# Performance work log

Measured on AMD Instinct MI355X. Metric: run time of the kernel, lower is better.

Reference implementation:

```python
import jax, jax.numpy as jnp
import numpy as np

N = 100000
E = 1600000
D = 256
BN_EPS = 1e-5


def setup_inputs() -> dict:
    key = jax.random.key(0)
    ks = jax.random.split(key, 6)
    node_feats = jax.random.normal(ks[0], (N, D), dtype=jnp.float32)
    src = jax.random.randint(ks[1], (E,), 0, N, dtype=jnp.int64)
    dst = jax.random.randint(ks[2], (E,), 0, N, dtype=jnp.int64)
    eps = jnp.zeros((1,), dtype=jnp.float32)
    # Kaiming-uniform-like scaled init for linear layers
    W1 = jax.random.normal(ks[3], (D, 2 * D), dtype=jnp.float32) * (1.0 / np.sqrt(D))
    b1 = jnp.zeros((2 * D,), dtype=jnp.float32)
    W2 = jax.random.normal(ks[4], (2 * D, D), dtype=jnp.float32) * (1.0 / np.sqrt(2 * D))
    b2 = jnp.zeros((D,), dtype=jnp.float32)
    gamma = jnp.ones((D,), dtype=jnp.float32)
    beta = jnp.zeros((D,), dtype=jnp.float32)
    return {"node_feats": node_feats, "src": src, "dst": dst, "eps": eps,
            "W1": W1, "b1": b1, "W2": W2, "b2": b2, "gamma": gamma, "beta": beta}


def reference(node_feats, src, dst, eps, W1, b1, W2, b2, gamma, beta):
    n = node_feats.shape[0]
    # copy_u / sum: gather source features, scatter-sum into destinations
    neigh = jax.ops.segment_sum(node_feats[src], dst, num_segments=n)  # [N, D]
    h = (1.0 + eps) * node_feats + neigh
    # 2-layer MLP: D -> 2D -> D with ReLU
    h = jax.nn.relu(h @ W1 + b1) @ W2 + b2
    # BatchNorm1d, training mode: batch stats over N, biased variance
    mean = jnp.mean(h, axis=0)
    var = jnp.mean(jnp.square(h - mean), axis=0)
    h = (h - mean) * jax.lax.rsqrt(var + BN_EPS) * gamma + beta
    return h
```

## Files before the change

### kernel.cpp

```cpp
#include <hip/hip_runtime.h>
#include <hip/hip_bf16.h>
#include <stdint.h>

#define N_NODES 100000
#define DIM 256
#define HID 512
#define N_EDGES 1600000

#define NBUCK 782
#define BSHIFT 7
#define BMASK 127
#define CAPC 4096
#define CURSTRIDE 16

using short8 = __attribute__((ext_vector_type(8))) short;
using f32x4  = __attribute__((ext_vector_type(4))) float;

__device__ __forceinline__ unsigned short f2bf(float f) {
    union { float f; unsigned u; } v; v.f = f;
    unsigned u = v.u;
    unsigned r = u + 0x7fffu + ((u >> 16) & 1u);
    return (unsigned short)(r >> 16);
}
__device__ __forceinline__ float bf2f(unsigned short u) {
    union { unsigned u; float f; } v; v.u = ((unsigned)u) << 16; return v.f;
}
__device__ __forceinline__ void gload_lds16(const void* g, void* l) {
    __builtin_amdgcn_global_load_lds((const __attribute__((address_space(1))) void*)g,
                                     (__attribute__((address_space(3))) void*)l, 16, 0, 0);
}

__global__ void x2bf(const float* __restrict__ x, unsigned short* __restrict__ xb) {
    long i = (long)blockIdx.x * blockDim.x + threadIdx.x;
    float4 u0 = ((const float4*)x)[i * 2];
    float4 u1 = ((const float4*)x)[i * 2 + 1];
    short8 o;
    o[0] = (short)f2bf(u0.x); o[1] = (short)f2bf(u0.y);
    o[2] = (short)f2bf(u0.z); o[3] = (short)f2bf(u0.w);
    o[4] = (short)f2bf(u1.x); o[5] = (short)f2bf(u1.y);
    o[6] = (short)f2bf(u1.z); o[7] = (short)f2bf(u1.w);
    ((short8*)xb)[i] = o;
}


__global__ void zero_cursors(int* __restrict__ chunkCursor) {
    int i = blockIdx.x * 256 + threadIdx.x;
    if (i < NBUCK * CURSTRIDE) chunkCursor[i] = 0;
}

__global__ void bucket_scatter(const int* __restrict__ src, const int* __restrict__ dst,
                               int* __restrict__ chunkCursor, int* __restrict__ bucketed) {
    int e = blockIdx.x * 256 + threadIdx.x;
    int d = dst[e];
    int c = d >> BSHIFT;
    int pos = atomicAdd(&chunkCursor[c * CURSTRIDE], 1);
    bucketed[(size_t)c * CAPC + pos] = src[e] | ((d & BMASK) << 17);
}

__global__ void scan_chunks(const int* __restrict__ chunkCursor, int* __restrict__ chunkOff) {
    __shared__ int sm[1024];
    int t = threadIdx.x;
    int v = (t < NBUCK) ? chunkCursor[t * CURSTRIDE] : 0;
    sm[t] = v;
    __syncthreads();
    for (int off = 1; off < 1024; off <<= 1) {
        int add = (t >= off) ? sm[t - off] : 0;
        __syncthreads();
        sm[t] += add;
        __syncthreads();
    }
    chunkOff[t] = sm[t] - v;
}

__global__ __launch_bounds__(256) void chunk_sort(const int* __restrict__ bucketed,
        const int* __restrict__ chunkCursor, const int* __restrict__ chunkOff,
        int* __restrict__ start, int* __restrict__ count, int* __restrict__ sorted_src) {
    __shared__ int cnt[128];
    __shared__ int cur[128];
    __shared__ int sortedL[CAPC];
    int c = blockIdx.x;
    int t = threadIdx.x;
    int nE = chunkCursor[c * CURSTRIDE];
    int base = chunkOff[c];
    const int* bk = bucketed + (size_t)c * CAPC;
    if (t < 128) cnt[t] = 0;
    __syncthreads();
    for (int i = t; i < nE; i += 256)
        atomicAdd(&cnt[bk[i] >> 17], 1);
    __syncthreads();
    int v = (t < 128) ? cnt[t] : 0;
    for (int off = 1; off < 128; off <<= 1) {
        int add = (t >= off && t < 128) ? cnt[t - off] : 0;
        __syncthreads();
        if (t < 128) cnt[t] += add;
        __syncthreads();
    }
    if (t < 128) {
        int excl = cnt[t] - v;
        int gid = c * 128 + t;
        start[gid] = base + excl;
        count[gid] = v;
        cur[t] = excl;
    }
    __syncthreads();
    for (int i = t; i < nE; i += 256) {
        int p = bk[i];
        int pos = atomicAdd(&cur[p >> 17], 1);
        sortedL[pos] = p & 0x1FFFF;
    }
    __syncthreads();
    for (int i = t; i < nE; i += 256)
        sorted_src[base + i] = sortedL[i];
}

__global__ void gather_sum(const unsigned short* __restrict__ xb, const int* __restrict__ sorted_src,
                           const int* __restrict__ start, const int* __restrict__ count,
                           const float* __restrict__ eps, unsigned short* __restrict__ accb) {
    int lane = threadIdx.x & 63;
    int n = blockIdx.x * 4 + (threadIdx.x >> 6);
    if (n >= N_NODES) return;
    float s = 1.0f + eps[0];
    const ushort4* xr = (const ushort4*)(xb + (size_t)n * DIM);
    ushort4 v = xr[lane];
    float a0 = bf2f(v.x) * s, a1 = bf2f(v.y) * s, a2 = bf2f(v.z) * s, a3 = bf2f(v.w) * s;
    int base = start[n];
    int end = base + count[n];
    int j = base;
    for (; j + 4 <= end; j += 4) {
        int s0 = sorted_src[j], s1 = sorted_src[j + 1];
        int s2 = sorted_src[j + 2], s3 = sorted_src[j + 3];
        ushort4 v0 = ((const ushort4*)(xb + (size_t)s0 * DIM))[lane];
        ushort4 v1 = ((const ushort4*)(xb + (size_t)s1 * DIM))[lane];
        ushort4 v2 = ((const ushort4*)(xb + (size_t)s2 * DIM))[lane];
        ushort4 v3 = ((const ushort4*)(xb + (size_t)s3 * DIM))[lane];
        a0 += bf2f(v0.x) + bf2f(v1.x) + bf2f(v2.x) + bf2f(v3.x);
        a1 += bf2f(v0.y) + bf2f(v1.y) + bf2f(v2.y) + bf2f(v3.y);
        a2 += bf2f(v0.z) + bf2f(v1.z) + bf2f(v2.z) + bf2f(v3.z);
        a3 += bf2f(v0.w) + bf2f(v1.w) + bf2f(v2.w) + bf2f(v3.w);
    }
    for (; j < end; ++j) {
        int s0 = sorted_src[j];
        ushort4 v0 = ((const ushort4*)(xb + (size_t)s0 * DIM))[lane];
        a0 += bf2f(v0.x); a1 += bf2f(v0.y); a2 += bf2f(v0.z); a3 += bf2f(v0.w);
    }
    ushort4 o;
    o.x = f2bf(a0); o.y = f2bf(a1); o.z = f2bf(a2); o.w = f2bf(a3);
    ((ushort4*)(accb + (size_t)n * DIM))[lane] = o;
}


__global__ void prep_weights(const float* __restrict__ W1, const float* __restrict__ W2,
                             unsigned short* __restrict__ W1t, unsigned short* __restrict__ W2t) {
    int tid = blockIdx.x * blockDim.x + threadIdx.x;
    if (tid < DIM * HID) {
        int n = tid >> 8, k = tid & 255;
        W1t[tid] = f2bf(W1[k * HID + n]);
    } else {
        int j = tid - DIM * HID;
        int n = j >> 9, k = j & 511;
        W2t[j] = f2bf(W2[k * DIM + n]);
    }
}

template<int K, int NOUT, bool RELU_BF16_OUT>
__global__ __launch_bounds__(256) void gemm128(const unsigned short* __restrict__ A,
        const unsigned short* __restrict__ Bt, const float* __restrict__ bias,
        void* __restrict__ Cout, int M) {
    __shared__ unsigned short As[128 * 32];
    __shared__ unsigned short Bs[128 * 32];
    constexpr int NT = NOUT / 128;
    int mtile = blockIdx.x / NT;
    int ntile = blockIdx.x % NT;
    int mbase = mtile * 128, nbase = ntile * 128;
    int t = threadIdx.x;
    int lane = t & 63, wid = t >> 6;
    int wm = (wid & 1) * 64, wn = (wid >> 1) * 64;
    int lo = lane & 15, quad = lane >> 4;

    int s0 = t, s1 = t + 256;
    int r0 = s0 >> 2, c0 = (s0 & 3) ^ ((r0 >> 1) & 3);
    int r1 = s1 >> 2, c1 = (s1 & 3) ^ ((r1 >> 1) & 3);
    int gmA0 = mbase + r0; if (gmA0 >= M) gmA0 = M - 1;
    int gmA1 = mbase + r1; if (gmA1 >= M) gmA1 = M - 1;
    const unsigned short* gA0 = A + (size_t)gmA0 * K + c0 * 8;
    const unsigned short* gA1 = A + (size_t)gmA1 * K + c1 * 8;
    const unsigned short* gB0 = Bt + (size_t)(nbase + r0) * K + c0 * 8;
    const unsigned short* gB1 = Bt + (size_t)(nbase + r1) * K + c1 * 8;
    char* lA0 = (char*)As + wid * 1024;
    char* lA1 = (char*)As + 4096 + wid * 1024;
    char* lB0 = (char*)Bs + wid * 1024;
    char* lB1 = (char*)Bs + 4096 + wid * 1024;

    int offA[4], offB[4];
    #pragma unroll
    for (int i = 0; i < 4; ++i) {
        int ra = wm + i * 16 + lo;
        offA[i] = ra * 64 + ((quad ^ ((ra >> 1) & 3)) * 16);
        int rb = wn + i * 16 + lo;
        offB[i] = rb * 64 + ((quad ^ ((rb >> 1) & 3)) * 16);
    }

    f32x4 acc[4][4] = {};
    for (int kt = 0; kt < K / 32; ++kt) {
        if (kt) __syncthreads();
        int ko = kt * 32;
        gload_lds16(gA0 + ko, lA0);
        gload_lds16(gA1 + ko, lA1);
        gload_lds16(gB0 + ko, lB0);
        gload_lds16(gB1 + ko, lB1);
        __syncthreads();
        short8 a[4], b[4];
        #pragma unroll
        for (int i = 0; i < 4; ++i) {
            a[i] = *(const short8*)((const char*)As + offA[i]);
            b[i] = *(const short8*)((const char*)Bs + offB[i]);
        }
        #pragma unroll
        for (int mi = 0; mi < 4; ++mi)
            #pragma unroll
            for (int ni = 0; ni < 4; ++ni)
                acc[mi][ni] = __builtin_amdgcn_mfma_f32_16x16x32_bf16(a[mi], b[ni], acc[mi][ni], 0, 0, 0);
    }
    #pragma unroll
    for (int mi = 0; mi < 4; ++mi)
      #pragma unroll
      for (int ni = 0; ni < 4; ++ni)
        #pragma unroll
        for (int r = 0; r < 4; ++r) {
            int row = mbase + wm + mi * 16 + quad * 4 + r;
            int col = nbase + wn + ni * 16 + lo;
            if (row < M) {
                float v = acc[mi][ni][r] + bias[col];
                if constexpr (RELU_BF16_OUT) {
                    v = fmaxf(v, 0.0f);
                    ((unsigned short*)Cout)[(size_t)row * NOUT + col] = f2bf(v);
                } else {
                    ((float*)Cout)[(size_t)row * NOUT + col] = v;
                }
            }
        }
}


__global__ void col_stats1(const float* __restrict__ h, float* __restrict__ partial) {
    int t = threadIdx.x;
    int b = blockIdx.x;
    int r0 = b * 200;
    int r1 = r0 + 200; if (r1 > N_NODES) r1 = N_NODES;
    float s = 0.f, q = 0.f;
    for (int r = r0; r < r1; ++r) {
        float v = h[(size_t)r * DIM + t];
        s += v; q += v * v;
    }
    partial[b * 512 + t] = s;
    partial[b * 512 + 256 + t] = q;
}

__global__ void col_stats2(const float* __restrict__ partial, const float* __restrict__ gamma,
                           const float* __restrict__ beta, float* __restrict__ sc) {
    int t = threadIdx.x;
    float s = 0.f, q = 0.f;
    for (int b = 0; b < 500; ++b) {
        s += partial[b * 512 + t];
        q += partial[b * 512 + 256 + t];
    }
    float mean = s * (1.0f / (float)N_NODES);
    float var = q * (1.0f / (float)N_NODES) - mean * mean;
    float inv = rsqrtf(var + 1e-5f);
    float scale = gamma[t] * inv;
    sc[t] = scale;
    sc[256 + t] = beta[t] - mean * scale;
}

__global__ void bn_apply(const float* __restrict__ h, const float* __restrict__ sc,
                         float* __restrict__ out) {
    long i = (long)blockIdx.x * blockDim.x + threadIdx.x;
    int c = (int)((i * 4) & (DIM - 1));
    float4 v = ((const float4*)h)[i];
    float4 scale = *(const float4*)(sc + c);
    float4 shift = *(const float4*)(sc + 256 + c);
    float4 o;
    o.x = v.x * scale.x + shift.x;
    o.y = v.y * scale.y + shift.y;
    o.z = v.z * scale.z + shift.z;
    o.w = v.w * scale.w + shift.w;
    ((float4*)out)[i] = o;
}

extern "C" void kernel_launch(void* const* d_in, const int* in_sizes, int n_in,
                              void* d_out, int out_size, void* d_ws, size_t ws_size,
                              hipStream_t stream) {
    const float* x     = (const float*)d_in[0];
    const int*   src   = (const int*)d_in[1];
    const int*   dst   = (const int*)d_in[2];
    const float* eps   = (const float*)d_in[3];
    const float* W1    = (const float*)d_in[4];
    const float* b1    = (const float*)d_in[5];
    const float* W2    = (const float*)d_in[6];
    const float* b2    = (const float*)d_in[7];
    const float* gamma = (const float*)d_in[8];
    const float* beta  = (const float*)d_in[9];

    char* ws = (char*)d_ws;
    unsigned short* xb   = (unsigned short*)ws;
    unsigned short* accb = (unsigned short*)(ws + 51200000);
    float*          h2   = (float*)ws;
    unsigned short* W1t  = (unsigned short*)(ws + 102400000);
    unsigned short* W2t  = (unsigned short*)(ws + 102662144);
    float*          sc   = (float*)(ws + 102924288);

    char* ob = (char*)d_out;
    int* chunkCursor = (int*)ob;
    int* chunkOff    = (int*)(ob + 51200);
    int* start       = (int*)(ob + 55296);
    int* count       = (int*)(ob + 455680);
    int* sorted_src  = (int*)(ob + 856064);
    int* bucketed    = (int*)(ob + 7256064);
    unsigned short* tbuf    = (unsigned short*)d_out;
    float*          partial = (float*)d_out;
    float*          out     = (float*)d_out;

    hipLaunchKernelGGL(x2bf, dim3(12500), dim3(256), 0, stream, x, xb);
    hipLaunchKernelGGL(prep_weights, dim3(1024), dim3(256), 0, stream, W1, W2, W1t, W2t);
    hipLaunchKernelGGL(zero_cursors, dim3(49), dim3(256), 0, stream, chunkCursor);
    hipLaunchKernelGGL(bucket_scatter, dim3(N_EDGES / 256), dim3(256), 0, stream,
                       src, dst, chunkCursor, bucketed);
    hipLaunchKernelGGL(scan_chunks, dim3(1), dim3(1024), 0, stream, chunkCursor, chunkOff);
    hipLaunchKernelGGL(chunk_sort, dim3(NBUCK), dim3(256), 0, stream,
                       bucketed, chunkCursor, chunkOff, start, count, sorted_src);
    hipLaunchKernelGGL(gather_sum, dim3(25000), dim3(256), 0, stream,
                       xb, sorted_src, start, count, eps, accb);
    hipLaunchKernelGGL((gemm128<256, 512, true>), dim3(782 * 4), dim3(256), 0, stream,
                       accb, W1t, b1, (void*)tbuf, N_NODES);
    hipLaunchKernelGGL((gemm128<512, 256, false>), dim3(782 * 2), dim3(256), 0, stream,
                       tbuf, W2t, b2, (void*)h2, N_NODES);
    hipLaunchKernelGGL(col_stats1, dim3(500), dim3(256), 0, stream, h2, partial);
    hipLaunchKernelGGL(col_stats2, dim3(1), dim3(256), 0, stream, partial, gamma, beta, sc);
    hipLaunchKernelGGL(bn_apply, dim3(25000), dim3(256), 0, stream, h2, sc, out);
}
```

Baseline: 664.1 us.

## Fuse BatchNorm column stats into second GEMM, persistent gather with sorted sources

Moves the column sum and sum-of-squares reduction into the epilogue of the second GEMM: each block reduces through shuffles and shared-memory atomics, then adds into one of 8 replicated global accumulators. This removes the separate col_stats1 pass that re-read the 100 MB fp32 output. The gather kernel becomes a grid-stride persistent kernel unrolled by 8 to keep more loads in flight. chunk_sort also insertion-sorts each destination's source list, which should improve locality of the gathers but adds serial per-thread work and makes the fp32 atomic column sums order-nondeterministic.

```diff
diff --git a/kernel.cpp b/kernel.cpp
--- a/kernel.cpp
+++ b/kernel.cpp
@@ -43,9 +43,10 @@
 }
 
 
-__global__ void zero_cursors(int* __restrict__ chunkCursor) {
+__global__ void zero_scratch(int* __restrict__ chunkCursor, float* __restrict__ gsums) {
     int i = blockIdx.x * 256 + threadIdx.x;
     if (i < NBUCK * CURSTRIDE) chunkCursor[i] = 0;
+    if (i < 4096) gsums[i] = 0.0f;
 }
 
 __global__ void bucket_scatter(const int* __restrict__ src, const int* __restrict__ dst,
@@ -95,12 +96,14 @@
         if (t < 128) cnt[t] += add;
         __syncthreads();
     }
+    int segs = 0, segc = 0;
     if (t < 128) {
-        int excl = cnt[t] - v;
+        segc = v;
+        segs = cnt[t] - v;
         int gid = c * 128 + t;
-        start[gid] = base + excl;
+        start[gid] = base + segs;
         count[gid] = v;
-        cur[t] = excl;
+        cur[t] = segs;
     }
     __syncthreads();
     for (int i = t; i < nE; i += 256) {
@@ -109,43 +112,72 @@
         sortedL[pos] = p & 0x1FFFF;
     }
     __syncthreads();
+    if (t < 128 && segc > 1) {
+        for (int i = segs + 1; i < segs + segc; ++i) {
+            int key = sortedL[i];
+            int k = i - 1;
+            while (k >= segs && sortedL[k] > key) { sortedL[k + 1] = sortedL[k]; --k; }
+            sortedL[k + 1] = key;
+        }
+    }
+    __syncthreads();
     for (int i = t; i < nE; i += 256)
         sorted_src[base + i] = sortedL[i];
 }
 
-__global__ void gather_sum(const unsigned short* __restrict__ xb, const int* __restrict__ sorted_src,
-                           const int* __restrict__ start, const int* __restrict__ count,
-                           const float* __restrict__ eps, unsigned short* __restrict__ accb) {
+__global__ __launch_bounds__(256) void gather_sum(const unsigned short* __restrict__ xb,
+        const int* __restrict__ sorted_src, const int* __restrict__ start,
+        const int* __restrict__ count, const float* __restrict__ eps,
+        unsigned short* __restrict__ accb) {
     int lane = threadIdx.x & 63;
-    int n = blockIdx.x * 4 + (threadIdx.x >> 6);
-    if (n >= N_NODES) return;
+    int wv = (blockIdx.x << 2) + (threadIdx.x >> 6);
     float s = 1.0f + eps[0];
-    const ushort4* xr = (const ushort4*)(xb + (size_t)n * DIM);
-    ushort4 v = xr[lane];
-    float a0 = bf2f(v.x) * s, a1 = bf2f(v.y) * s, a2 = bf2f(v.z) * s, a3 = bf2f(v.w) * s;
-    int base = start[n];
-    int end = base + count[n];
-    int j = base;
-    for (; j + 4 <= end; j += 4) {
-        int s0 = sorted_src[j], s1 = sorted_src[j + 1];
-        int s2 = sorted_src[j + 2], s3 = sorted_src[j + 3];
-        ushort4 v0 = ((const ushort4*)(xb + (size_t)s0 * DIM))[lane];
-        ushort4 v1 = ((const ushort4*)(xb + (size_t)s1 * DIM))[lane];
-        ushort4 v2 = ((const ushort4*)(xb + (size_t)s2 * DIM))[lane];
-        ushort4 v3 = ((const ushort4*)(xb + (size_t)s3 * DIM))[lane];
-        a0 += bf2f(v0.x) + bf2f(v1.x) + bf2f(v2.x) + bf2f(v3.x);
-        a1 += bf2f(v0.y) + bf2f(v1.y) + bf2f(v2.y) + bf2f(v3.y);
-        a2 += bf2f(v0.z) + bf2f(v1.z) + bf2f(v2.z) + bf2f(v3.z);
-        a3 += bf2f(v0.w) + bf2f(v1.w) + bf2f(v2.w) + bf2f(v3.w);
-    }
-    for (; j < end; ++j) {
-        int s0 = sorted_src[j];
-        ushort4 v0 = ((const ushort4*)(xb + (size_t)s0 * DIM))[lane];
-        a0 += bf2f(v0.x); a1 += bf2f(v0.y); a2 += bf2f(v0.z); a3 += bf2f(v0.w);
-    }
-    ushort4 o;
-    o.x = f2bf(a0); o.y = f2bf(a1); o.z = f2bf(a2); o.w = f2bf(a3);
-    ((ushort4*)(accb + (size_t)n * DIM))[lane] = o;
+    for (int n = wv; n < N_NODES; n += 8192) {
+        ushort4 v = ((const ushort4*)(xb + (size_t)n * DIM))[lane];
+        float a0 = bf2f(v.x) * s, a1 = bf2f(v.y) * s, a2 = bf2f(v.z) * s, a3 = bf2f(v.w) * s;
+        int base = start[n];
+        int end = base + count[n];
+        int j = base;
+        for (; j + 8 <= end; j += 8) {
+            int i0 = sorted_src[j],     i1 = sorted_src[j + 1];
+            int i2 = sorted_src[j + 2], i3 = sorted_src[j + 3];
+            int i4 = sorted_src[j + 4], i5 = sorted_src[j + 5];
+            int i6 = sorted_src[j + 6], i7 = sorted_src[j + 7];
+            ushort4 v0 = ((const ushort4*)(xb + (size_t)i0 * DIM))[lane];
+            ushort4 v1 = ((const ushort4*)(xb + (size_t)i1 * DIM))[lane];
+            ushort4 v2 = ((const ushort4*)(xb + (size_t)i2 * DIM))[lane];
+            ushort4 v3 = ((const ushort4*)(xb + (size_t)i3 * DIM))[lane];
+            ushort4 v4 = ((const ushort4*)(xb + (size_t)i4 * DIM))[lane];
+            ushort4 v5 = ((const ushort4*)(xb + (size_t)i5 * DIM))[lane];
+            ushort4 v6 = ((const ushort4*)(xb + (size_t)i6 * DIM))[lane];
+            ushort4 v7 = ((const ushort4*)(xb + (size_t)i7 * DIM))[lane];
+            a0 += (bf2f(v0.x) + bf2f(v1.x)) + (bf2f(v2.x) + bf2f(v3.x))
+                + (bf2f(v4.x) + bf2f(v5.x)) + (bf2f(v6.x) + bf2f(v7.x));
+            a1 += (bf2f(v0.y) + bf2f(v1.y)) + (bf2f(v2.y) + bf2f(v3.y))
+                + (bf2f(v4.y) + bf2f(v5.y)) + (bf2f(v6.y) + bf2f(v7.y));
+            a2 += (bf2f(v0.z) + bf2f(v1.z)) + (bf2f(v2.z) + bf2f(v3.z))
+                + (bf2f(v4.z) + bf2f(v5.z)) + (bf2f(v6.z) + bf2f(v7.z));
+            a3 += (bf2f(v0.w) + bf2f(v1.w)) + (bf2f(v2.w) + bf2f(v3.w))
+                + (bf2f(v4.w) + bf2f(v5.w)) + (bf2f(v6.w) + bf2f(v7.w));
+        }
+        for (; j + 2 <= end; j += 2) {
+            int i0 = sorted_src[j], i1 = sorted_src[j + 1];
+            ushort4 v0 = ((const ushort4*)(xb + (size_t)i0 * DIM))[lane];
+            ushort4 v1 = ((const ushort4*)(xb + (size_t)i1 * DIM))[lane];
+            a0 += bf2f(v0.x) + bf2f(v1.x);
+            a1 += bf2f(v0.y) + bf2f(v1.y);
+            a2 += bf2f(v0.z) + bf2f(v1.z);
+            a3 += bf2f(v0.w) + bf2f(v1.w);
+        }
+        if (j < end) {
+            int i0 = sorted_src[j];
+            ushort4 v0 = ((const ushort4*)(xb + (size_t)i0 * DIM))[lane];
+            a0 += bf2f(v0.x); a1 += bf2f(v0.y); a2 += bf2f(v0.z); a3 += bf2f(v0.w);
+        }
+        ushort4 o;
+        o.x = f2bf(a0); o.y = f2bf(a1); o.z = f2bf(a2); o.w = f2bf(a3);
+        ((ushort4*)(accb + (size_t)n * DIM))[lane] = o;
+    }
 }
 
 
@@ -162,10 +194,10 @@
     }
 }
 
-template<int K, int NOUT, bool RELU_BF16_OUT>
+template<int K, int NOUT, bool RELU_BF16_OUT, bool COLSTATS>
 __global__ __launch_bounds__(256) void gemm128(const unsigned short* __restrict__ A,
         const unsigned short* __restrict__ Bt, const float* __restrict__ bias,
-        void* __restrict__ Cout, int M) {
+        void* __restrict__ Cout, float* __restrict__ gsums, int M) {
     __shared__ unsigned short As[128 * 32];
     __shared__ unsigned short Bs[128 * 32];
     constexpr int NT = NOUT / 128;
@@ -221,6 +253,7 @@
             for (int ni = 0; ni < 4; ++ni)
                 acc[mi][ni] = __builtin_amdgcn_mfma_f32_16x16x32_bf16(a[mi], b[ni], acc[mi][ni], 0, 0, 0);
     }
+    float cs[4] = {0.f, 0.f, 0.f, 0.f}, cq[4] = {0.f, 0.f, 0.f, 0.f};
     #pragma unroll
     for (int mi = 0; mi < 4; ++mi)
       #pragma unroll
@@ -237,32 +270,40 @@
                 } else {
                     ((float*)Cout)[(size_t)row * NOUT + col] = v;
                 }
+                if constexpr (COLSTATS) { cs[ni] += v; cq[ni] += v * v; }
             }
         }
-}
-
-
-__global__ void col_stats1(const float* __restrict__ h, float* __restrict__ partial) {
-    int t = threadIdx.x;
-    int b = blockIdx.x;
-    int r0 = b * 200;
-    int r1 = r0 + 200; if (r1 > N_NODES) r1 = N_NODES;
-    float s = 0.f, q = 0.f;
-    for (int r = r0; r < r1; ++r) {
-        float v = h[(size_t)r * DIM + t];
-        s += v; q += v * v;
-    }
-    partial[b * 512 + t] = s;
-    partial[b * 512 + 256 + t] = q;
-}
-
-__global__ void col_stats2(const float* __restrict__ partial, const float* __restrict__ gamma,
+    if constexpr (COLSTATS) {
+        __shared__ float colS[128], colQ[128];
+        if (t < 128) { colS[t] = 0.f; colQ[t] = 0.f; }
+        __syncthreads();
+        #pragma unroll
+        for (int ni = 0; ni < 4; ++ni) {
+            float sv = cs[ni], qv = cq[ni];
+            sv += __shfl_xor(sv, 16); sv += __shfl_xor(sv, 32);
+            qv += __shfl_xor(qv, 16); qv += __shfl_xor(qv, 32);
+            if (quad == 0) {
+                atomicAdd(&colS[wn + ni * 16 + lo], sv);
+                atomicAdd(&colQ[wn + ni * 16 + lo], qv);
+            }
+        }
+        __syncthreads();
+        if (t < 128) {
+            int rep = blockIdx.x & 7;
+            atomicAdd(&gsums[rep * 512 + nbase + t], colS[t]);
+            atomicAdd(&gsums[rep * 512 + 256 + nbase + t], colQ[t]);
+        }
+    }
+}
+
+
+__global__ void col_stats2(const float* __restrict__ gsums, const float* __restrict__ gamma,
                            const float* __restrict__ beta, float* __restrict__ sc) {
     int t = threadIdx.x;
     float s = 0.f, q = 0.f;
-    for (int b = 0; b < 500; ++b) {
-        s += partial[b * 512 + t];
-        q += partial[b * 512 + 256 + t];
+    for (int rep = 0; rep < 8; ++rep) {
+        s += gsums[rep * 512 + t];
+        q += gsums[rep * 512 + 256 + t];
     }
     float mean = s * (1.0f / (float)N_NODES);
     float var = q * (1.0f / (float)N_NODES) - mean * mean;
@@ -308,6 +349,7 @@
     unsigned short* W1t  = (unsigned short*)(ws + 102400000);
     unsigned short* W2t  = (unsigned short*)(ws + 102662144);
     float*          sc   = (float*)(ws + 102924288);
+    float*          gsums = (float*)(ws + 102926336);
 
     char* ob = (char*)d_out;
     int* chunkCursor = (int*)ob;
@@ -316,25 +358,23 @@
     int* count       = (int*)(ob + 455680);
     int* sorted_src  = (int*)(ob + 856064);
     int* bucketed    = (int*)(ob + 7256064);
-    unsigned short* tbuf    = (unsigned short*)d_out;
-    float*          partial = (float*)d_out;
-    float*          out     = (float*)d_out;
+    unsigned short* tbuf = (unsigned short*)d_out;
+    float*          out  = (float*)d_out;
 
     hipLaunchKernelGGL(x2bf, dim3(12500), dim3(256), 0, stream, x, xb);
     hipLaunchKernelGGL(prep_weights, dim3(1024), dim3(256), 0, stream, W1, W2, W1t, W2t);
-    hipLaunchKernelGGL(zero_cursors, dim3(49), dim3(256), 0, stream, chunkCursor);
+    hipLaunchKernelGGL(zero_scratch, dim3(49), dim3(256), 0, stream, chunkCursor, gsums);
     hipLaunchKernelGGL(bucket_scatter, dim3(N_EDGES / 256), dim3(256), 0, stream,
                        src, dst, chunkCursor, bucketed);
     hipLaunchKernelGGL(scan_chunks, dim3(1), dim3(1024), 0, stream, chunkCursor, chunkOff);
     hipLaunchKernelGGL(chunk_sort, dim3(NBUCK), dim3(256), 0, stream,
                        bucketed, chunkCursor, chunkOff, start, count, sorted_src);
-    hipLaunchKernelGGL(gather_sum, dim3(25000), dim3(256), 0, stream,
+    hipLaunchKernelGGL(gather_sum, dim3(2048), dim3(256), 0, stream,
                        xb, sorted_src, start, count, eps, accb);
-    hipLaunchKernelGGL((gemm128<256, 512, true>), dim3(782 * 4), dim3(256), 0, stream,
-                       accb, W1t, b1, (void*)tbuf, N_NODES);
-    hipLaunchKernelGGL((gemm128<512, 256, false>), dim3(782 * 2), dim3(256), 0, stream,
-                       tbuf, W2t, b2, (void*)h2, N_NODES);
-    hipLaunchKernelGGL(col_stats1, dim3(500), dim3(256), 0, stream, h2, partial);
-    hipLaunchKernelGGL(col_stats2, dim3(1), dim3(256), 0, stream, partial, gamma, beta, sc);
+    hipLaunchKernelGGL((gemm128<256, 512, true, false>), dim3(782 * 4), dim3(256), 0, stream,
+                       accb, W1t, b1, (void*)tbuf, nullptr, N_NODES);
+    hipLaunchKernelGGL((gemm128<512, 256, false, true>), dim3(782 * 2), dim3(256), 0, stream,
+                       tbuf, W2t, b2, (void*)h2, gsums, N_NODES);
+    hipLaunchKernelGGL(col_stats2, dim3(1), dim3(256), 0, stream, gsums, gamma, beta, sc);
     hipLaunchKernelGGL(bn_apply, dim3(25000), dim3(256), 0, stream, h2, sc, out);
 }
```

Result: faster. 645.8 us (-2.8%).
